# Optimization experiments

Hardware: AMD Instinct MI355X
Metric: run time of the kernel (lower is better)

## Reference

```python
import jax, jax.numpy as jnp
import numpy as np

H, D = 16, 64  # heads, head dim; E = H*D


def setup_inputs() -> dict:
    key = jax.random.key(0)
    ks = jax.random.split(key, 8)
    B, T, E = 4, 1024, 1024
    s = (2.0 / E) ** 0.5
    return {
        "x": jax.random.normal(ks[0], (B, T, E), jnp.float32),
        "wq": jax.random.normal(ks[1], (H * D, E), jnp.float32) * s,
        "wk": jax.random.normal(ks[2], (H * D, E), jnp.float32) * s,
        "wv": jax.random.normal(ks[3], (H * D, E), jnp.float32) * s,
        "wvr": jax.random.normal(ks[4], (H * D, E), jnp.float32) * s,
        "wr": jax.random.normal(ks[5], (H, E, T), jnp.float32) * s,
        "wj": jax.random.normal(ks[6], (E, E), jnp.float32) * s,
        "gate": jnp.zeros((H, 3), jnp.float32),
        "wo": jax.random.normal(ks[7], (E, H * D), jnp.float32) * s,
    }


def reference(x, wq, wk, wv, wvr, wr, wj, gate, wo):
    B, T, E = x.shape
    scale = 1.0 / D ** 0.5

    def proj(w):  # torch Linear: y = x @ w.T, then split heads -> (B,H,T,D)
        return jnp.einsum('bte,fe->btf', x, w).reshape(B, T, H, D).transpose(0, 2, 1, 3)

    mask = jnp.triu(jnp.ones((T, T), bool), 1)  # True above diagonal (masked)

    # --- branch 1: standard causal QKV attention ---
    q, k, v = proj(wq), proj(wk), proj(wv)
    s1 = jnp.einsum('bhid,bhjd->bhij', q, k) * scale
    a1 = jax.nn.softmax(jnp.where(mask, -jnp.inf, s1), axis=-1)
    out1 = jnp.einsum('bhij,bhjd->bhid', a1, v)

    # --- branch 2: RRPRAM (parameter-based per-key scores, broadcast over queries) ---
    rv = proj(wvr)
    s2 = jnp.einsum('bte,het->bht', x, wr[:, :, :T]) * scale  # score per key position
    s2 = jnp.broadcast_to(s2[:, :, None, :], (B, H, T, T))
    a2 = jax.nn.softmax(jnp.where(mask, -jnp.inf, s2), axis=-1)
    out2 = jnp.einsum('bhij,bhjd->bhid', a2, rv)

    # --- branch 3: Janus self-echo (rank-1 outer-product scores) ---
    echo = jnp.einsum('bte,fe->btf', x, wj)            # x @ wj.T
    echo_back = jnp.einsum('btf,fe->bte', echo, wj)    # echo @ wj
    sc = jnp.sum(x * echo_back, axis=-1) / (E ** 0.5)  # (B,T)
    s3 = sc[:, :, None] * sc[:, None, :]               # (B,T,T)
    a3 = jax.nn.softmax(jnp.where(mask, -jnp.inf, s3), axis=-1)
    jv = echo.reshape(B, T, H, D).transpose(0, 2, 1, 3)
    out3 = jnp.einsum('bij,bhjd->bhid', a3, jv)

    # --- gated combine (softmax over the 3 branches per head) ---
    g = jax.nn.softmax(gate, axis=-1)  # (H,3)
    out = (g[:, 0][None, :, None, None] * out1
           + g[:, 1][None, :, None, None] * out2
           + g[:, 2][None, :, None, None] * out3)
    out = out.transpose(0, 2, 1, 3).reshape(B, T, H * D)
    return jnp.einsum('btf,ef->bte', out, wo)
```

## Files before the change

### kernel.cpp

```cpp
#include <hip/hip_runtime.h>
#include <cstdint>
#include <cstddef>

typedef unsigned short u16;
typedef short bf16x8 __attribute__((ext_vector_type(8)));
typedef short bf16x4 __attribute__((ext_vector_type(4)));
typedef float f32x4 __attribute__((ext_vector_type(4)));

constexpr int B_ = 4, T_ = 1024, E_ = 1024, H_ = 16, D_ = 64;

__device__ __forceinline__ float bf2f(u16 u) {
  union { unsigned u; float f; } v; v.u = ((unsigned)u) << 16; return v.f;
}
__device__ __forceinline__ u16 f2bf(float f) {
  union { float f; unsigned u; } v; v.f = f;
  return (u16)((v.u + 0x7fffu + ((v.u >> 16) & 1u)) >> 16);
}

#define GLD_LDS16(gp, lp)                                                      \
  __builtin_amdgcn_global_load_lds(                                            \
      (const __attribute__((address_space(1))) void*)(gp),                     \
      (__attribute__((address_space(3))) void*)(lp), 16, 0, 0)

#define SBAR()                                                                 \
  do {                                                                         \
    __builtin_amdgcn_sched_barrier(0);                                         \
    __builtin_amdgcn_s_barrier();                                              \
    __builtin_amdgcn_sched_barrier(0);                                         \
  } while (0)
#define WAIT_LGKM0()                                                           \
  do {                                                                         \
    asm volatile("s_waitcnt lgkmcnt(0)" ::: "memory");                         \
    __builtin_amdgcn_sched_barrier(0);                                         \
  } while (0)
#define WAIT_VM6()                                                             \
  do {                                                                         \
    asm volatile("s_waitcnt vmcnt(6)" ::: "memory");                           \
    __builtin_amdgcn_sched_barrier(0);                                         \
  } while (0)

__global__ __launch_bounds__(512) void gemm_qkv8(
    const u16* __restrict__ A, const u16* __restrict__ Bm, u16* __restrict__ C)
{
  __shared__ u16 smem[65536];

  const int tid  = threadIdx.x;
  const int lane = tid & 63;
  const int wave = tid >> 6;
  const int wm = wave >> 2;
  const int wn = wave & 3;
  const int fr = lane & 15;
  const int fg = lane >> 4;
  const int fx = fr & 7;
  const int m0 = blockIdx.y * 256;
  const int n0 = blockIdx.x * 256;

  auto stage = [&](int g) {
    const int half = g & 3;
    const int buf  = (g >> 2) & 1;
    int kt = g >> 2; if (kt > 15) kt = 15;
    const int k0 = kt << 6;
    const u16* src = (half < 2)
        ? (A  + (size_t)(m0 + (half & 1) * 128) * 1024)
        : (Bm + (size_t)(n0 + (half & 1) * 128) * 1024);
    u16* dst = smem + (buf << 15) + (half << 13);
    #pragma unroll
    for (int l = 0; l < 2; l++) {
      const int s = (l << 9) | tid;
      const int r = s >> 3, ch = s & 7;
      GLD_LDS16(src + (size_t)r * 1024 + k0 + ((ch ^ (r & 7)) << 3), dst + s * 8);
    }
  };

  f32x4 acc[8][4];
  #pragma unroll
  for (int i = 0; i < 8; i++)
    #pragma unroll
    for (int j = 0; j < 4; j++) acc[i][j] = f32x4{0.f, 0.f, 0.f, 0.f};

  #pragma unroll
  for (int g = 0; g < 7; g++) stage(g);
  WAIT_VM6();
  __builtin_amdgcn_s_barrier();
  __builtin_amdgcn_sched_barrier(0);

  const int ko0 = (fg ^ fx) << 3;
  const int ko1 = ((4 | fg) ^ fx) << 3;

  bf16x8 aF[8][2], bF[4][2];

  #pragma unroll 2
  for (int t = 0; t < 16; t++) {
    const int buf = t & 1;
    const int ab = (buf << 15) + (wm << 13) + fr * 64;
    const int bb = (buf << 15) + 16384 + ((wn >> 1) << 13) + ((wn & 1) << 12) + fr * 64;

    #pragma unroll
    for (int mt = 0; mt < 8; mt++) {
      aF[mt][0] = *(const bf16x8*)(smem + ab + mt * 1024 + ko0);
      aF[mt][1] = *(const bf16x8*)(smem + ab + mt * 1024 + ko1);
    }
    #pragma unroll
    for (int nt = 0; nt < 2; nt++) {
      bF[nt][0] = *(const bf16x8*)(smem + bb + nt * 1024 + ko0);
      bF[nt][1] = *(const bf16x8*)(smem + bb + nt * 1024 + ko1);
    }
    stage(4 * t + 7);
    SBAR();
    WAIT_LGKM0();
    __builtin_amdgcn_s_setprio(1);
    #pragma unroll
    for (int mt = 0; mt < 4; mt++)
      #pragma unroll
      for (int nt = 0; nt < 2; nt++) {
        acc[mt][nt] = __builtin_amdgcn_mfma_f32_16x16x32_bf16(aF[mt][0], bF[nt][0], acc[mt][nt], 0, 0, 0);
        acc[mt][nt] = __builtin_amdgcn_mfma_f32_16x16x32_bf16(aF[mt][1], bF[nt][1], acc[mt][nt], 0, 0, 0);
      }
    __builtin_amdgcn_s_setprio(0);
    SBAR();

    #pragma unroll
    for (int nt = 2; nt < 4; nt++) {
      bF[nt][0] = *(const bf16x8*)(smem + bb + nt * 1024 + ko0);
      bF[nt][1] = *(const bf16x8*)(smem + bb + nt * 1024 + ko1);
    }
    stage(4 * t + 8);
    SBAR();
    WAIT_LGKM0();
    __builtin_amdgcn_s_setprio(1);
    #pragma unroll
    for (int mt = 0; mt < 4; mt++)
      #pragma unroll
      for (int nt = 2; nt < 4; nt++) {
        acc[mt][nt] = __builtin_amdgcn_mfma_f32_16x16x32_bf16(aF[mt][0], bF[nt][0], acc[mt][nt], 0, 0, 0);
        acc[mt][nt] = __builtin_amdgcn_mfma_f32_16x16x32_bf16(aF[mt][1], bF[nt][1], acc[mt][nt], 0, 0, 0);
      }
    __builtin_amdgcn_s_setprio(0);
    SBAR();

    stage(4 * t + 9);
    SBAR();
    __builtin_amdgcn_s_setprio(1);
    #pragma unroll
    for (int mt = 4; mt < 8; mt++)
      #pragma unroll
      for (int nt = 0; nt < 2; nt++) {
        acc[mt][nt] = __builtin_amdgcn_mfma_f32_16x16x32_bf16(aF[mt][0], bF[nt][0], acc[mt][nt], 0, 0, 0);
        acc[mt][nt] = __builtin_amdgcn_mfma_f32_16x16x32_bf16(aF[mt][1], bF[nt][1], acc[mt][nt], 0, 0, 0);
      }
    __builtin_amdgcn_s_setprio(0);
    SBAR();

    stage(4 * t + 10);
    SBAR();
    __builtin_amdgcn_s_setprio(1);
    #pragma unroll
    for (int mt = 4; mt < 8; mt++)
      #pragma unroll
      for (int nt = 2; nt < 4; nt++) {
        acc[mt][nt] = __builtin_amdgcn_mfma_f32_16x16x32_bf16(aF[mt][0], bF[nt][0], acc[mt][nt], 0, 0, 0);
        acc[mt][nt] = __builtin_amdgcn_mfma_f32_16x16x32_bf16(aF[mt][1], bF[nt][1], acc[mt][nt], 0, 0, 0);
      }
    __builtin_amdgcn_s_setprio(0);
    WAIT_VM6();
    __builtin_amdgcn_s_barrier();
    __builtin_amdgcn_sched_barrier(0);
  }

  u16* Cp = C + (size_t)(m0 + wm * 128) * 4096 + n0 + wn * 64;
  #pragma unroll
  for (int mt = 0; mt < 8; mt++)
    #pragma unroll
    for (int nt = 0; nt < 4; nt++)
      #pragma unroll
      for (int r2 = 0; r2 < 4; r2++)
        Cp[(size_t)(mt * 16 + fg * 4 + r2) * 4096 + nt * 16 + fr] = f2bf(acc[mt][nt][r2]);
}

template<int WM, int WN, int MT, int NT, bool CBF16>
__global__ __launch_bounds__(WM * WN * 64) void gemm_bt(
    const u16* __restrict__ A, const u16* __restrict__ Bm,
    void* __restrict__ Cv, int N, int K,
    int lda, int ldb, int ldc,
    long batchA, long batchB, long batchC, float alpha)
{
  constexpr int TM = WM * MT * 16;
  constexpr int TN = WN * NT * 16;
  constexpr int THREADS = WM * WN * 64;
  constexpr int ASZ = TM * 32, BSZ = TN * 32;

  __shared__ u16 smem[ASZ + BSZ];
  u16* sA = smem;
  u16* sB = smem + ASZ;

  const int z = blockIdx.z;
  const u16* Ab = A + (size_t)z * batchA;
  const u16* Bb = Bm + (size_t)z * batchB;
  const int m0 = blockIdx.y * TM;
  const int n0 = blockIdx.x * TN;
  const int tid = threadIdx.x;
  const int lane = tid & 63;
  const int wave = tid >> 6;
  const int wm = wave % WM;
  const int wn = wave / WM;
  const int fr = lane & 15;
  const int fg = lane >> 4;

  f32x4 acc[MT][NT];
  const f32x4 zero = {0.f, 0.f, 0.f, 0.f};
  #pragma unroll
  for (int i = 0; i < MT; i++)
    #pragma unroll
    for (int j = 0; j < NT; j++) acc[i][j] = zero;

  for (int k0 = 0; k0 < K; k0 += 32) {
    __syncthreads();
    for (int s = tid; s < TM * 4; s += THREADS) {
      const int row = s >> 2, ch = s & 3;
      GLD_LDS16(Ab + (size_t)(m0 + row) * lda + k0 + ch * 8, &sA[s * 8]);
    }
    for (int s = tid; s < TN * 4; s += THREADS) {
      const int row = s >> 2, ch = s & 3;
      int rr = n0 + row; if (rr > N - 1) rr = N - 1;
      GLD_LDS16(Bb + (size_t)rr * ldb + k0 + ch * 8, &sB[s * 8]);
    }
    __syncthreads();

    bf16x8 av[MT], bv[NT];
    #pragma unroll
    for (int mt = 0; mt < MT; mt++)
      av[mt] = *(const bf16x8*)&sA[((wm * MT + mt) * 16 + fr) * 32 + fg * 8];
    #pragma unroll
    for (int nt = 0; nt < NT; nt++)
      bv[nt] = *(const bf16x8*)&sB[((wn * NT + nt) * 16 + fr) * 32 + fg * 8];
    #pragma unroll
    for (int mt = 0; mt < MT; mt++)
      #pragma unroll
      for (int nt = 0; nt < NT; nt++)
        acc[mt][nt] = __builtin_amdgcn_mfma_f32_16x16x32_bf16(av[mt], bv[nt], acc[mt][nt], 0, 0, 0);
  }

  const int er = (lane >> 4) * 4;
  const int ec = lane & 15;
  #pragma unroll
  for (int mt = 0; mt < MT; mt++) {
    #pragma unroll
    for (int nt = 0; nt < NT; nt++) {
      const int row = m0 + (wm * MT + mt) * 16 + er;
      const int col = n0 + (wn * NT + nt) * 16 + ec;
      if (col < N) {
        #pragma unroll
        for (int r2 = 0; r2 < 4; r2++) {
          const float vv = acc[mt][nt][r2] * alpha;
          const size_t ci = (size_t)z * batchC + (size_t)(row + r2) * ldc + col;
          if constexpr (CBF16) ((u16*)Cv)[ci] = f2bf(vv);
          else                 ((float*)Cv)[ci] = vv;
        }
      }
    }
  }
}

__global__ __launch_bounds__(256) void gemm_echo(
    const u16* __restrict__ A, const u16* __restrict__ Alo,
    const u16* __restrict__ Bm, const u16* __restrict__ Blo,
    u16* __restrict__ echoT, float* __restrict__ sc)
{
  constexpr int TM = 128, TN = 64;
  constexpr int ASZ = TM * 32, BSZ = TN * 32;
  __shared__ u16 smem[2 * (ASZ + BSZ)];
  u16* sA  = smem;
  u16* sB  = smem + ASZ;
  u16* sAl = smem + ASZ + BSZ;
  u16* sBl = smem + 2 * ASZ + BSZ;

  const int m0 = blockIdx.y * TM;
  const int n0 = blockIdx.x * TN;
  const int tid = threadIdx.x;
  const int lane = tid & 63;
  const int wave = tid >> 6;
  const int wm = wave % 2;
  const int wn = wave / 2;
  const int fr = lane & 15, fg = lane >> 4;

  f32x4 acc[4][2];
  #pragma unroll
  for (int i = 0; i < 4; i++)
    #pragma unroll
    for (int j = 0; j < 2; j++) acc[i][j] = f32x4{0.f, 0.f, 0.f, 0.f};

  for (int k0 = 0; k0 < E_; k0 += 32) {
    __syncthreads();
    for (int s = tid; s < TM * 4; s += 256) {
      const int row = s >> 2, ch = s & 3;
      const size_t go = (size_t)(m0 + row) * E_ + k0 + ch * 8;
      GLD_LDS16(A + go, &sA[s * 8]);
      GLD_LDS16(Alo + go, &sAl[s * 8]);
    }
    for (int s = tid; s < TN * 4; s += 256) {
      const int row = s >> 2, ch = s & 3;
      const size_t go = (size_t)(n0 + row) * E_ + k0 + ch * 8;
      GLD_LDS16(Bm + go, &sB[s * 8]);
      GLD_LDS16(Blo + go, &sBl[s * 8]);
    }
    __syncthreads();

    bf16x8 av[4], bv[2], al[4], bl[2];
    #pragma unroll
    for (int mt = 0; mt < 4; mt++) {
      av[mt] = *(const bf16x8*)&sA[((wm * 4 + mt) * 16 + fr) * 32 + fg * 8];
      al[mt] = *(const bf16x8*)&sAl[((wm * 4 + mt) * 16 + fr) * 32 + fg * 8];
    }
    #pragma unroll
    for (int nt = 0; nt < 2; nt++) {
      bv[nt] = *(const bf16x8*)&sB[((wn * 2 + nt) * 16 + fr) * 32 + fg * 8];
      bl[nt] = *(const bf16x8*)&sBl[((wn * 2 + nt) * 16 + fr) * 32 + fg * 8];
    }
    #pragma unroll
    for (int mt = 0; mt < 4; mt++)
      #pragma unroll
      for (int nt = 0; nt < 2; nt++) {
        acc[mt][nt] = __builtin_amdgcn_mfma_f32_16x16x32_bf16(av[mt], bv[nt], acc[mt][nt], 0, 0, 0);
        acc[mt][nt] = __builtin_amdgcn_mfma_f32_16x16x32_bf16(al[mt], bv[nt], acc[mt][nt], 0, 0, 0);
        acc[mt][nt] = __builtin_amdgcn_mfma_f32_16x16x32_bf16(av[mt], bl[nt], acc[mt][nt], 0, 0, 0);
      }
  }

  __syncthreads();
  const int b   = m0 >> 10;
  const int t0l = m0 & 1023;
  const int ec  = lane & 15;
  u16* lt = smem;

  #pragma unroll
  for (int mt = 0; mt < 4; mt++) {
    float sq[4] = {0.f, 0.f, 0.f, 0.f};
    #pragma unroll
    for (int nt = 0; nt < 2; nt++) {
      const int cl = (wn * 2 + nt) * 16 + ec;
      #pragma unroll
      for (int r2 = 0; r2 < 4; r2++) {
        const float vv = acc[mt][nt][r2];
        sq[r2] += vv * vv;
        lt[cl * 132 + (wm * 4 + mt) * 16 + fg * 4 + r2] = f2bf(vv);
      }
    }
    #pragma unroll
    for (int m2 = 1; m2 < 16; m2 <<= 1) {
      sq[0] += __shfl_xor(sq[0], m2, 64);
      sq[1] += __shfl_xor(sq[1], m2, 64);
      sq[2] += __shfl_xor(sq[2], m2, 64);
      sq[3] += __shfl_xor(sq[3], m2, 64);
    }
    if (ec == 0) {
      #pragma unroll
      for (int r2 = 0; r2 < 4; r2++)
        atomicAdd(&sc[(size_t)b * T_ + t0l + (wm * 4 + mt) * 16 + fg * 4 + r2], sq[r2]);
    }
  }
  __syncthreads();
  for (int s = tid; s < 64 * 128; s += 256) {
    const int f = s >> 7, t = s & 127;
    echoT[((size_t)b * E_ + n0 + f) * T_ + t0l + t] = lt[f * 132 + t];
  }
}

__global__ __launch_bounds__(256, 2) void flash1(
    const u16* __restrict__ qkvr, const u16* __restrict__ vTb, u16* __restrict__ out1) {
  const int it = blockIdx.x, h = blockIdx.y, b = blockIdx.z;
  const int tid = threadIdx.x, lane = tid & 63, w = tid >> 6;
  const int fr = lane & 15, fg = lane >> 4;

  __shared__ u16 sQ[8192];
  __shared__ u16 sK[8192];
  __shared__ u16 sV[8192];

  const u16* Qb = qkvr + ((size_t)(b * T_) + it * 128) * 4096 + h * 64;
  const u16* Kb = qkvr + (size_t)(b * T_) * 4096 + 1024 + h * 64;
  const u16* Vb = vTb + (size_t)(b * H_ + h) * (D_ * T_);

  for (int s = tid; s < 1024; s += 256) {
    const int l = s & 63, g = s >> 6;
    const int row = (g >> 1) * 16 + (l & 15);
    const int c8  = (g & 1) * 4 + (l >> 4);
    GLD_LDS16(Qb + (size_t)row * 4096 + c8 * 8, &sQ[s * 8]);
  }
  __syncthreads();

  bf16x8 bQ[2][2];
  #pragma unroll
  for (int mf = 0; mf < 2; mf++)
    #pragma unroll
    for (int kk = 0; kk < 2; kk++)
      bQ[mf][kk] = *(const bf16x8*)&sQ[((((w * 2 + mf) * 2 + kk) << 6) | lane) * 8];

  f32x4 accO[2][4];
  float mrow[2], lrow[2];
  #pragma unroll
  for (int mf = 0; mf < 2; mf++) {
    mrow[mf] = -3.0e38f; lrow[mf] = 0.f;
    #pragma unroll
    for (int nd = 0; nd < 4; nd++) accO[mf][nd] = f32x4{0.f, 0.f, 0.f, 0.f};
  }

  for (int jt = 0; jt <= it; jt++) {
    __syncthreads();
    for (int s = tid; s < 1024; s += 256) {
      const int l = s & 63, g = s >> 6;
      const int row = (g >> 1) * 16 + (l & 15);
      const int c8  = (g & 1) * 4 + (l >> 4);
      GLD_LDS16(Kb + (size_t)(jt * 128 + row) * 4096 + c8 * 8, &sK[s * 8]);
    }
    for (int s = tid; s < 1024; s += 256) {
      const int jc = s >> 6, d = s & 63;
      GLD_LDS16(Vb + ((size_t)(jt * 16 + jc)) * 512 + d * 8, &sV[s * 8]);
    }
    __syncthreads();

    f32x4 accST[2][8];
    #pragma unroll
    for (int mf = 0; mf < 2; mf++)
      #pragma unroll
      for (int nf = 0; nf < 8; nf++) accST[mf][nf] = f32x4{0.f, 0.f, 0.f, 0.f};
    #pragma unroll
    for (int kk = 0; kk < 2; kk++) {
      #pragma unroll
      for (int nf = 0; nf < 8; nf++) {
        const bf16x8 aK = *(const bf16x8*)&sK[((((nf << 1) | kk) << 6) | lane) * 8];
        accST[0][nf] = __builtin_amdgcn_mfma_f32_16x16x32_bf16(aK, bQ[0][kk], accST[0][nf], 0, 0, 0);
        accST[1][nf] = __builtin_amdgcn_mfma_f32_16x16x32_bf16(aK, bQ[1][kk], accST[1][nf], 0, 0, 0);
      }
    }

    const bool diag = (jt == it);
    bf16x4 pf[2][8];
    #pragma unroll
    for (int mf = 0; mf < 2; mf++) {
      const int iloc = w * 32 + mf * 16 + fr;
      float sv[8][4];
      float rmax = -3.0e38f;
      #pragma unroll
      for (int nf = 0; nf < 8; nf++)
        #pragma unroll
        for (int r = 0; r < 4; r++) {
          float s = accST[mf][nf][r] * 0.125f;
          if (diag && (nf * 16 + fg * 4 + r) > iloc) s = -3.0e38f;
          sv[nf][r] = s;
          rmax = fmaxf(rmax, s);
        }
      rmax = fmaxf(rmax, __shfl_xor(rmax, 16, 64));
      rmax = fmaxf(rmax, __shfl_xor(rmax, 32, 64));
      const float mn = fmaxf(mrow[mf], rmax);
      const float al = __expf(mrow[mf] - mn);
      mrow[mf] = mn;
      float ps = 0.f;
      #pragma unroll
      for (int nf = 0; nf < 8; nf++)
        #pragma unroll
        for (int r = 0; r < 4; r++) {
          const float pv = __expf(sv[nf][r] - mn);
          ps += pv;
          pf[mf][nf][r] = (short)f2bf(pv);
        }
      ps += __shfl_xor(ps, 16, 64);
      ps += __shfl_xor(ps, 32, 64);
      lrow[mf] = lrow[mf] * al + ps;
      #pragma unroll
      for (int r = 0; r < 4; r++) {
        const float alr = __shfl(al, fg * 4 + r, 64);
        #pragma unroll
        for (int nd = 0; nd < 4; nd++) accO[mf][nd][r] *= alr;
      }
    }

    #pragma unroll
    for (int kc = 0; kc < 8; kc++) {
      bf16x8 bV[4];
      #pragma unroll
      for (int nd = 0; nd < 4; nd++) {
        const bf16x4 vv = *(const bf16x4*)&sV[
            (((kc * 2 + (fg >> 1)) * 64 + nd * 16 + fr) * 8) + (fg & 1) * 4];
        bV[nd] = bf16x8{vv[0], vv[1], vv[2], vv[3], 0, 0, 0, 0};
      }
      #pragma unroll
      for (int mf = 0; mf < 2; mf++) {
        const bf16x4 pp = pf[mf][kc];
        const bf16x8 pA = bf16x8{pp[0], pp[1], pp[2], pp[3], 0, 0, 0, 0};
        #pragma unroll
        for (int nd = 0; nd < 4; nd++)
          accO[mf][nd] = __builtin_amdgcn_mfma_f32_16x16x32_bf16(pA, bV[nd], accO[mf][nd], 0, 0, 0);
      }
    }
  }

  u16* op = out1 + ((size_t)(b * T_) + it * 128) * E_ + h * 64;
  #pragma unroll
  for (int mf = 0; mf < 2; mf++) {
    const float li = 1.0f / lrow[mf];
    #pragma unroll
    for (int r = 0; r < 4; r++) {
      const float linv = __shfl(li, fg * 4 + r, 64);
      const int row = w * 32 + mf * 16 + fg * 4 + r;
      #pragma unroll
      for (int nd = 0; nd < 4; nd++)
        op[(size_t)row * E_ + nd * 16 + fr] = f2bf(accO[mf][nd][r] * linv);
    }
  }
}

__device__ __forceinline__ float block_max256(float v, float* red) {
  #pragma unroll
  for (int m = 32; m > 0; m >>= 1) v = fmaxf(v, __shfl_xor(v, m, 64));
  if ((threadIdx.x & 63) == 0) red[threadIdx.x >> 6] = v;
  __syncthreads();
  const float r = fmaxf(fmaxf(red[0], red[1]), fmaxf(red[2], red[3]));
  __syncthreads();
  return r;
}
__device__ __forceinline__ float block_sum256(float v, float* red) {
  #pragma unroll
  for (int m = 32; m > 0; m >>= 1) v += __shfl_xor(v, m, 64);
  if ((threadIdx.x & 63) == 0) red[threadIdx.x >> 6] = v;
  __syncthreads();
  const float r = (red[0] + red[1]) + (red[2] + red[3]);
  __syncthreads();
  return r;
}

__global__ __launch_bounds__(256) void cast_all(
    const float* __restrict__ x, const float* __restrict__ wq,
    const float* __restrict__ wk, const float* __restrict__ wv,
    const float* __restrict__ wvr, const float* __restrict__ wo,
    const float* __restrict__ wj,
    u16* __restrict__ xb, u16* __restrict__ xlo, u16* __restrict__ wcat,
    u16* __restrict__ wob, u16* __restrict__ wjb, u16* __restrict__ wjlo) {
  const int bid = blockIdx.x;
  if (bid < 4096) {
    const size_t i = ((size_t)bid * 256 + threadIdx.x) * 4;
    const float4 v = *(const float4*)(x + i);
    ushort4 oh, ol;
    oh.x = f2bf(v.x); ol.x = f2bf(v.x - bf2f(oh.x));
    oh.y = f2bf(v.y); ol.y = f2bf(v.y - bf2f(oh.y));
    oh.z = f2bf(v.z); ol.z = f2bf(v.z - bf2f(oh.z));
    oh.w = f2bf(v.w); ol.w = f2bf(v.w - bf2f(oh.w));
    *(ushort4*)(xb + i) = oh;
    *(ushort4*)(xlo + i) = ol;
  } else if (bid < 8192) {
    const int r = (bid - 4096) >> 10;
    const float* src = (r == 0) ? wq : (r == 1) ? wk : (r == 2) ? wv : wvr;
    const size_t i = ((size_t)((bid - 4096) & 1023) * 256 + threadIdx.x) * 4;
    const float4 v = *(const float4*)(src + i);
    ushort4 o;
    o.x = f2bf(v.x); o.y = f2bf(v.y); o.z = f2bf(v.z); o.w = f2bf(v.w);
    *(ushort4*)(wcat + (size_t)r * (1 << 20) + i) = o;
  } else if (bid < 9216) {
    const size_t i = ((size_t)(bid - 8192) * 256 + threadIdx.x) * 4;
    const float4 v = *(const float4*)(wo + i);
    ushort4 o;
    o.x = f2bf(v.x); o.y = f2bf(v.y); o.z = f2bf(v.z); o.w = f2bf(v.w);
    *(ushort4*)(wob + i) = o;
  } else {
    const size_t i = ((size_t)(bid - 9216) * 256 + threadIdx.x) * 4;
    const float4 v = *(const float4*)(wj + i);
    ushort4 oh, ol;
    oh.x = f2bf(v.x); ol.x = f2bf(v.x - bf2f(oh.x));
    oh.y = f2bf(v.y); ol.y = f2bf(v.y - bf2f(oh.y));
    oh.z = f2bf(v.z); ol.z = f2bf(v.z - bf2f(oh.z));
    oh.w = f2bf(v.w); ol.w = f2bf(v.w - bf2f(oh.w));
    *(ushort4*)(wjb + i) = oh;
    *(ushort4*)(wjlo + i) = ol;
  }
}

__global__ __launch_bounds__(256) void s2_direct(
    const u16* __restrict__ xb, const float* __restrict__ wr, float* __restrict__ s2) {
  const int t0 = blockIdx.x * 32, h = blockIdx.y;
  const int tt = threadIdx.x & 31, eg = threadIdx.x >> 5;
  float acc[4] = {0.f, 0.f, 0.f, 0.f};
  const float* wp = wr + (size_t)h * E_ * T_ + t0 + tt;
  for (int ec = 0; ec < 8; ec++) {
    const int e0 = ec * 128 + eg * 16;
    bf16x8 xv[4][2];
    #pragma unroll
    for (int b = 0; b < 4; b++) {
      const u16* xp = xb + ((size_t)(b * T_) + t0 + tt) * E_ + e0;
      xv[b][0] = *(const bf16x8*)xp;
      xv[b][1] = *(const bf16x8*)(xp + 8);
    }
    #pragma unroll
    for (int e2 = 0; e2 < 16; e2++) {
      const float w = wp[(size_t)(e0 + e2) * T_];
      #pragma unroll
      for (int b = 0; b < 4; b++)
        acc[b] += bf2f((u16)xv[b][e2 >> 3][e2 & 7]) * w;
    }
  }
  __shared__ float red[8][4][33];
  #pragma unroll
  for (int b = 0; b < 4; b++) red[eg][b][tt] = acc[b];
  __syncthreads();
  if (threadIdx.x < 128) {
    const int b = threadIdx.x >> 5, t = threadIdx.x & 31;
    float s = 0.f;
    #pragma unroll
    for (int g = 0; g < 8; g++) s += red[g][b][t];
    s2[((size_t)b * H_ + h) * T_ + t0 + t] = s * 0.125f;
  }
}

__global__ __launch_bounds__(256) void a3_softmax(const float* __restrict__ sc, u16* __restrict__ a3) {
  const int i = blockIdx.x;
  const int b = blockIdx.y;
  const float* sr = sc + (size_t)b * T_;
  const float sci = sr[i] * 0.03125f;
  u16* row = a3 + ((size_t)b * T_ + i) * T_;
  __shared__ float red[4];
  float v[4];
  float m = -3.0e38f;
  #pragma unroll
  for (int k = 0; k < 4; k++) {
    const int j = threadIdx.x + k * 256;
    const float xv = (j <= i) ? sci * (sr[j] * 0.03125f) : -3.0e38f;
    v[k] = xv;
    m = fmaxf(m, xv);
  }
  m = block_max256(m, red);
  float s = 0.f;
  #pragma unroll
  for (int k = 0; k < 4; k++) {
    const int j = threadIdx.x + k * 256;
    const float p = (j <= i) ? __expf(v[k] - m) : 0.f;
    v[k] = p;
    s += p;
  }
  s = block_sum256(s, red);
  const float inv = 1.0f / s;
  #pragma unroll
  for (int k = 0; k < 4; k++) {
    const int j = threadIdx.x + k * 256;
    row[j] = f2bf(v[k] * inv);
  }
}

__global__ __launch_bounds__(1024) void branch2_scan(
    const float* __restrict__ s2, const u16* __restrict__ rv, int ldrv,
    u16* __restrict__ out2) {
  const int h = blockIdx.x, b = blockIdx.y;
  const int tid = threadIdx.x;
  const int lane = tid & 63;
  const int wv = tid >> 6;

  const float* srow = s2 + ((size_t)b * H_ + h) * T_;

  __shared__ float wbuf[T_];
  __shared__ float numtot[16][64];
  __shared__ float dentot[16];
  __shared__ float redm[16];

  float m = srow[tid];
  #pragma unroll
  for (int mk = 32; mk > 0; mk >>= 1) m = fmaxf(m, __shfl_xor(m, mk, 64));
  if (lane == 0) redm[wv] = m;
  __syncthreads();
  m = redm[0];
  #pragma unroll
  for (int i2 = 1; i2 < 16; i2++) m = fmaxf(m, redm[i2]);

  wbuf[tid] = __expf(srow[tid] - m);
  __syncthreads();

  const u16* rvp = rv + (size_t)(b * T_) * ldrv + h * D_ + lane;
  const int j0 = wv * 64;
  float num = 0.f, den = 0.f;
  #pragma unroll 8
  for (int j2 = 0; j2 < 64; j2++) {
    const float w = wbuf[j0 + j2];
    den += w;
    num += w * bf2f(rvp[(size_t)(j0 + j2) * ldrv]);
  }
  numtot[wv][lane] = num;
  if (lane == 0) dentot[wv] = den;
  __syncthreads();

  float num_off = 0.f, den_off = 0.f;
  for (int w2 = 0; w2 < wv; w2++) {
    num_off += numtot[w2][lane];
    den_off += dentot[w2];
  }

  u16* op = out2 + (size_t)b * T_ * E_ + h * D_ + lane;
  num = num_off; den = den_off;
  #pragma unroll 8
  for (int j2 = 0; j2 < 64; j2++) {
    const float w = wbuf[j0 + j2];
    num += w * bf2f(rvp[(size_t)(j0 + j2) * ldrv]);
    den += w;
    op[(size_t)(j0 + j2) * E_] = f2bf(num / den);
  }
}

__global__ __launch_bounds__(256) void transpose_v(const u16* __restrict__ v, u16* __restrict__ vTb,
                                                   int ldv) {
  const int bh = blockIdx.x;
  const int b = bh >> 4, h = bh & 15;
  const int d0 = blockIdx.y * 32, t0 = blockIdx.z * 32;
  __shared__ u16 tile[32][33];
  const int c = threadIdx.x & 31, r0 = threadIdx.x >> 5;
  #pragma unroll
  for (int rr = 0; rr < 32; rr += 8) {
    const int t = t0 + rr + r0;
    tile[rr + r0][c] = v[((size_t)b * T_ + t) * ldv + h * 64 + d0 + c];
  }
  __syncthreads();
  #pragma unroll
  for (int rr = 0; rr < 32; rr += 8) {
    const int d = d0 + rr + r0;
    const int t = t0 + c;
    vTb[((size_t)(bh * 128 + (t >> 3)) * 64 + d) * 8 + (t & 7)] = tile[c][rr + r0];
  }
}

__global__ __launch_bounds__(256) void combine_gate(
    const u16* __restrict__ o1, const u16* __restrict__ o2, const u16* __restrict__ o3,
    const float* __restrict__ gate, u16* __restrict__ comb) {
  const size_t idx = (size_t)blockIdx.x * 256 + threadIdx.x;
  const int f = (int)(idx & (E_ - 1));
  const int h = f >> 6;
  const float g0 = gate[h * 3 + 0], g1 = gate[h * 3 + 1], g2 = gate[h * 3 + 2];
  const float mx = fmaxf(g0, fmaxf(g1, g2));
  const float e0 = __expf(g0 - mx), e1 = __expf(g1 - mx), e2 = __expf(g2 - mx);
  const float inv = 1.0f / (e0 + e1 + e2);
  const float o = (e0 * bf2f(o1[idx]) + e1 * bf2f(o2[idx]) + e2 * bf2f(o3[idx])) * inv;
  comb[idx] = f2bf(o);
}

extern "C" void kernel_launch(void* const* d_in, const int* in_sizes, int n_in,
                              void* d_out, int out_size, void* d_ws, size_t ws_size,
                              hipStream_t stream) {
  (void)in_sizes; (void)n_in; (void)out_size; (void)ws_size;
  const float* x    = (const float*)d_in[0];
  const float* wq   = (const float*)d_in[1];
  const float* wk   = (const float*)d_in[2];
  const float* wv   = (const float*)d_in[3];
  const float* wvr  = (const float*)d_in[4];
  const float* wr   = (const float*)d_in[5];
  const float* wj   = (const float*)d_in[6];
  const float* gate = (const float*)d_in[7];
  const float* wo   = (const float*)d_in[8];
  float* out = (float*)d_out;

  char* p = (char*)d_ws;
  auto alloc = [&](size_t bytes) -> char* {
    char* r = p; p += (bytes + 255) & ~(size_t)255; return r;
  };
  const size_t NTE = (size_t)B_ * T_ * E_;
  const size_t NW  = (size_t)E_ * E_;

  u16* xb    = (u16*)alloc(NTE * 2);
  u16* xlo   = (u16*)alloc(NTE * 2);
  u16* wcat  = (u16*)alloc(4 * NW * 2);
  u16* wjb   = (u16*)alloc(NW * 2);
  u16* wjlo  = (u16*)alloc(NW * 2);
  u16* wob   = (u16*)alloc(NW * 2);
  u16* qkvr  = (u16*)alloc(NTE * 4 * 2);
  u16* vT    = (u16*)alloc(NTE * 2);
  u16* echoT = (u16*)alloc(NTE * 2);
  u16* a3p   = (u16*)alloc(NTE * 2);
  float* sc  = (float*)alloc((size_t)B_ * T_ * 4);
  float* s2  = (float*)alloc((size_t)B_ * H_ * T_ * 4);
  u16* out1b = (u16*)alloc(NTE * 2);
  u16* out2b = (u16*)alloc(NTE * 2);
  u16* out3b = (u16*)alloc(NTE * 2);
  u16* comb  = (u16*)alloc(NTE * 2);

  cast_all<<<dim3(10240), 256, 0, stream>>>(x, wq, wk, wv, wvr, wo, wj,
                                            xb, xlo, wcat, wob, wjb, wjlo);
  hipMemsetAsync(sc, 0, (size_t)B_ * T_ * 4, stream);

  gemm_qkv8<<<dim3(16, 16), 512, 0, stream>>>(xb, wcat, qkvr);

  gemm_echo<<<dim3(16, 32, 1), 256, 0, stream>>>(xb, xlo, wjb, wjlo, echoT, sc);

  transpose_v<<<dim3(B_ * H_, D_ / 32, T_ / 32), 256, 0, stream>>>(qkvr + 2048, vT, 4096);
  s2_direct<<<dim3(T_ / 32, H_), 256, 0, stream>>>(xb, wr, s2);

  branch2_scan<<<dim3(H_, B_), 1024, 0, stream>>>(s2, qkvr + 3072, 4096, out2b);

  a3_softmax<<<dim3(T_, B_), 256, 0, stream>>>(sc, a3p);
  gemm_bt<2,2,4,2,true><<<dim3(E_ / 64, T_ / 128, B_), 256, 0, stream>>>(
      a3p, echoT, out3b, E_, T_, T_, T_, E_,
      (long)T_ * T_, (long)E_ * T_, (long)T_ * E_, 1.f);

  flash1<<<dim3(T_ / 128, H_, B_), 256, 0, stream>>>(qkvr, vT, out1b);

  combine_gate<<<dim3((unsigned)(NTE / 256)), 256, 0, stream>>>(out1b, out2b, out3b, gate, comb);
  gemm_bt<2,2,4,2,false><<<dim3(E_ / 64, (B_ * T_) / 128, 1), 256, 0, stream>>>(
      comb, wob, out, E_, E_, E_, E_, E_, 0L, 0L, 0L, 1.f);
}
```

Baseline: 388.7 us.

## Cut register use in QKV GEMM to fit two blocks per CU

The QKV projection GEMM now loads A fragments in two halves of four tiles instead of all eight, shrinking the live register set. It requests two 512-thread blocks per CU through launch bounds. The global-to-LDS staging order is reworked to match a per-quarter phase schedule, with a shallower prefetch depth (vmcnt 4 instead of 6). The aim is higher occupancy to hide latency, at the cost of extra LDS reads and less prefetch lookahead. 128KB of LDS per block may also stop two blocks from co-residing on a CU.

```diff
diff --git a/kernel.cpp b/kernel.cpp
--- a/kernel.cpp
+++ b/kernel.cpp
@@ -33,13 +33,13 @@
     asm volatile("s_waitcnt lgkmcnt(0)" ::: "memory");                         \
     __builtin_amdgcn_sched_barrier(0);                                         \
   } while (0)
-#define WAIT_VM6()                                                             \
+#define WAIT_VM4()                                                             \
   do {                                                                         \
-    asm volatile("s_waitcnt vmcnt(6)" ::: "memory");                           \
+    asm volatile("s_waitcnt vmcnt(4)" ::: "memory");                           \
     __builtin_amdgcn_sched_barrier(0);                                         \
   } while (0)
 
-__global__ __launch_bounds__(512) void gemm_qkv8(
+__global__ __launch_bounds__(512, 2) void gemm_qkv8(
     const u16* __restrict__ A, const u16* __restrict__ Bm, u16* __restrict__ C)
 {
   __shared__ u16 smem[65536];
@@ -55,10 +55,9 @@
   const int m0 = blockIdx.y * 256;
   const int n0 = blockIdx.x * 256;
 
-  auto stage = [&](int g) {
-    const int half = g & 3;
-    const int buf  = (g >> 2) & 1;
-    int kt = g >> 2; if (kt > 15) kt = 15;
+  auto stage = [&](int ktl, int half) {
+    const int buf = ktl & 1;
+    int kt = (ktl > 15) ? 15 : ktl;
     const int k0 = kt << 6;
     const u16* src = (half < 2)
         ? (A  + (size_t)(m0 + (half & 1) * 128) * 1024)
@@ -78,25 +77,24 @@
     #pragma unroll
     for (int j = 0; j < 4; j++) acc[i][j] = f32x4{0.f, 0.f, 0.f, 0.f};
 
-  #pragma unroll
-  for (int g = 0; g < 7; g++) stage(g);
-  WAIT_VM6();
+  stage(0, 0); stage(0, 1); stage(0, 2); stage(0, 3);
+  stage(1, 2); stage(1, 0);
+  WAIT_VM4();
   __builtin_amdgcn_s_barrier();
   __builtin_amdgcn_sched_barrier(0);
 
   const int ko0 = (fg ^ fx) << 3;
   const int ko1 = ((4 | fg) ^ fx) << 3;
 
-  bf16x8 aF[8][2], bF[4][2];
-
-  #pragma unroll 2
   for (int t = 0; t < 16; t++) {
     const int buf = t & 1;
     const int ab = (buf << 15) + (wm << 13) + fr * 64;
-    const int bb = (buf << 15) + 16384 + ((wn >> 1) << 13) + ((wn & 1) << 12) + fr * 64;
-
-    #pragma unroll
-    for (int mt = 0; mt < 8; mt++) {
+    const int bb = (buf << 15) + 16384 + (wn << 12) + fr * 64;
+
+    bf16x8 aF[4][2], bF[4][2];
+
+    #pragma unroll
+    for (int mt = 0; mt < 4; mt++) {
       aF[mt][0] = *(const bf16x8*)(smem + ab + mt * 1024 + ko0);
       aF[mt][1] = *(const bf16x8*)(smem + ab + mt * 1024 + ko1);
     }
@@ -105,7 +103,7 @@
       bF[nt][0] = *(const bf16x8*)(smem + bb + nt * 1024 + ko0);
       bF[nt][1] = *(const bf16x8*)(smem + bb + nt * 1024 + ko1);
     }
-    stage(4 * t + 7);
+    stage(t + 1, 1);
     SBAR();
     WAIT_LGKM0();
     __builtin_amdgcn_s_setprio(1);
@@ -124,7 +122,7 @@
       bF[nt][0] = *(const bf16x8*)(smem + bb + nt * 1024 + ko0);
       bF[nt][1] = *(const bf16x8*)(smem + bb + nt * 1024 + ko1);
     }
-    stage(4 * t + 8);
+    stage(t + 1, 3);
     SBAR();
     WAIT_LGKM0();
     __builtin_amdgcn_s_setprio(1);
@@ -138,31 +136,37 @@
     __builtin_amdgcn_s_setprio(0);
     SBAR();
 
-    stage(4 * t + 9);
+    #pragma unroll
+    for (int mt = 0; mt < 4; mt++) {
+      aF[mt][0] = *(const bf16x8*)(smem + ab + (4 + mt) * 1024 + ko0);
+      aF[mt][1] = *(const bf16x8*)(smem + ab + (4 + mt) * 1024 + ko1);
+    }
+    stage(t + 2, 2);
+    SBAR();
+    WAIT_LGKM0();
+    __builtin_amdgcn_s_setprio(1);
+    #pragma unroll
+    for (int mt = 0; mt < 4; mt++)
+      #pragma unroll
+      for (int nt = 0; nt < 2; nt++) {
+        acc[4 + mt][nt] = __builtin_amdgcn_mfma_f32_16x16x32_bf16(aF[mt][0], bF[nt][0], acc[4 + mt][nt], 0, 0, 0);
+        acc[4 + mt][nt] = __builtin_amdgcn_mfma_f32_16x16x32_bf16(aF[mt][1], bF[nt][1], acc[4 + mt][nt], 0, 0, 0);
+      }
+    __builtin_amdgcn_s_setprio(0);
+    SBAR();
+
+    stage(t + 2, 0);
     SBAR();
     __builtin_amdgcn_s_setprio(1);
     #pragma unroll
-    for (int mt = 4; mt < 8; mt++)
-      #pragma unroll
-      for (int nt = 0; nt < 2; nt++) {
-        acc[mt][nt] = __builtin_amdgcn_mfma_f32_16x16x32_bf16(aF[mt][0], bF[nt][0], acc[mt][nt], 0, 0, 0);
-        acc[mt][nt] = __builtin_amdgcn_mfma_f32_16x16x32_bf16(aF[mt][1], bF[nt][1], acc[mt][nt], 0, 0, 0);
+    for (int mt = 0; mt < 4; mt++)
+      #pragma unroll
+      for (int nt = 2; nt < 4; nt++) {
+        acc[4 + mt][nt] = __builtin_amdgcn_mfma_f32_16x16x32_bf16(aF[mt][0], bF[nt][0], acc[4 + mt][nt], 0, 0, 0);
+        acc[4 + mt][nt] = __builtin_amdgcn_mfma_f32_16x16x32_bf16(aF[mt][1], bF[nt][1], acc[4 + mt][nt], 0, 0, 0);
       }
     __builtin_amdgcn_s_setprio(0);
-    SBAR();
-
-    stage(4 * t + 10);
-    SBAR();
-    __builtin_amdgcn_s_setprio(1);
-    #pragma unroll
-    for (int mt = 4; mt < 8; mt++)
-      #pragma unroll
-      for (int nt = 2; nt < 4; nt++) {
-        acc[mt][nt] = __builtin_amdgcn_mfma_f32_16x16x32_bf16(aF[mt][0], bF[nt][0], acc[mt][nt], 0, 0, 0);
-        acc[mt][nt] = __builtin_amdgcn_mfma_f32_16x16x32_bf16(aF[mt][1], bF[nt][1], acc[mt][nt], 0, 0, 0);
-      }
-    __builtin_amdgcn_s_setprio(0);
-    WAIT_VM6();
+    WAIT_VM4();
     __builtin_amdgcn_s_barrier();
     __builtin_amdgcn_sched_barrier(0);
   }
```

Measured after the change: 375.9 us. -3.3%, faster.
